# Performance work log

Hardware: AMD Instinct MI355X
Metric: run time of the kernel (lower is better)

The kernel has to match this reference:

```python
import jax, jax.numpy as jnp
import numpy as np

EMB = 768
HEADS = 12
HEAD_DIM = EMB // HEADS  # 64
SCALE = 1.0 / float(np.sqrt(EMB))  # NOTE: source divides by sqrt(emb_size), not sqrt(head_dim)


def setup_inputs() -> dict:
    key = jax.random.key(0)
    k_x, k_wqkv, k_bqkv, k_wp, k_bp = jax.random.split(key, 5)
    b, n = 4, 2048
    x = jax.random.normal(k_x, (b, n, EMB), dtype=jnp.float32)
    # torch Linear default init ~ U(-1/sqrt(in), 1/sqrt(in)); scale doesn't matter for correctness baseline
    lim = 1.0 / np.sqrt(EMB)
    W_qkv = jax.random.uniform(k_wqkv, (EMB, 3 * EMB), minval=-lim, maxval=lim, dtype=jnp.float32)
    b_qkv = jax.random.uniform(k_bqkv, (3 * EMB,), minval=-lim, maxval=lim, dtype=jnp.float32)
    W_proj = jax.random.uniform(k_wp, (EMB, EMB), minval=-lim, maxval=lim, dtype=jnp.float32)
    b_proj = jax.random.uniform(k_bp, (EMB,), minval=-lim, maxval=lim, dtype=jnp.float32)
    return {"x": x, "W_qkv": W_qkv, "b_qkv": b_qkv, "W_proj": W_proj, "b_proj": b_proj}


def reference(x, W_qkv, b_qkv, W_proj, b_proj):
    b, n, _ = x.shape
    qkv = x @ W_qkv + b_qkv                              # [b, n, 3*emb]
    # rearrange 'b n (h d qkv) -> qkv b h n d' : qkv is the innermost split
    qkv = qkv.reshape(b, n, HEADS, HEAD_DIM, 3)
    qkv = jnp.transpose(qkv, (4, 0, 2, 1, 3))            # [3, b, h, n, d]
    q, k, v = qkv[0], qkv[1], qkv[2]
    att = jnp.einsum('bhnd,bhmd->bhnm', q, k) * SCALE    # [b, h, n, n]
    att = jax.nn.softmax(att, axis=-1)
    # dropout is identity at inference
    out = jnp.einsum('bhnm,bhmd->bhnd', att, v)          # [b, h, n, d]
    out = jnp.transpose(out, (0, 2, 1, 3)).reshape(b, n, EMB)  # 'b h n d -> b n (h d)'
    return out @ W_proj + b_proj
```

## Files before the change

### kernel.cpp

```cpp
#include <hip/hip_runtime.h>
#include <math.h>

typedef _Float16 f16x8 __attribute__((ext_vector_type(8)));
typedef _Float16 f16x4 __attribute__((ext_vector_type(4)));
typedef float f32x4 __attribute__((ext_vector_type(4)));
typedef unsigned int uint32;
typedef unsigned short ushort16;

static constexpr int EMB_ = 768;
static constexpr int NH_ = 12;
static constexpr int HD_ = 64;
static constexpr int SEQ_ = 2048;
static constexpr int B_ = 4;
static constexpr float QSCALE_ = 0.036084391824351615f * 1.4426950408889634f;

__device__ __forceinline__ void gload_lds16(const void* g, void* l) {
    __builtin_amdgcn_global_load_lds((const __attribute__((address_space(1))) void*)g,
                                     (__attribute__((address_space(3))) void*)l,
                                     16, 0, 0);
}

__global__ __launch_bounds__(256)
void prep_k(const float* __restrict__ W0, _Float16* __restrict__ Wt0,
            const float* __restrict__ W1, _Float16* __restrict__ Wt1,
            const float* __restrict__ x, _Float16* __restrict__ xh,
            int C0, int C1, int n4)
{
    const int tid = threadIdx.x;
    if (blockIdx.z == 2) {
        const int stride = 72 * 24 * 256;
        for (int i = (blockIdx.y * 72 + blockIdx.x) * 256 + tid; i < n4; i += stride) {
            float4 v = ((const float4*)x)[i];
            f16x4 o = {(_Float16)v.x, (_Float16)v.y, (_Float16)v.z, (_Float16)v.w};
            ((f16x4*)xh)[i] = o;
        }
        return;
    }
    const float* W; _Float16* Wt; int C;
    if (blockIdx.z == 0) { W = W0; Wt = Wt0; C = C0; }
    else                 { W = W1; Wt = Wt1; C = C1; }
    const int c0 = blockIdx.x * 32;
    if (c0 >= C) return;
    const int r0 = blockIdx.y * 32;
    __shared__ float ls[32][33];
    const int tc = tid & 31, tr = tid >> 5;
#pragma unroll
    for (int i = 0; i < 4; ++i)
        ls[tr + 8 * i][tc] = W[(size_t)(r0 + tr + 8 * i) * C + c0 + tc];
    __syncthreads();
#pragma unroll
    for (int i = 0; i < 4; ++i)
        Wt[(size_t)(c0 + tr + 8 * i) * EMB_ + r0 + tc] = (_Float16)ls[tc][tr + 8 * i];
}

template<int EPI>
__global__ __launch_bounds__(256, 2)
void gemm16(const _Float16* __restrict__ A, const _Float16* __restrict__ Bt,
            const float* __restrict__ bias, float* __restrict__ outF,
            _Float16* __restrict__ hq, _Float16* __restrict__ hk,
            _Float16* __restrict__ hv,
            int M, int N, int K)
{
    __shared__ __align__(16) _Float16 As[128 * 64];
    __shared__ __align__(16) _Float16 Bs[128 * 64];

    const int tid  = threadIdx.x;
    const int lane = tid & 63;
    const int w    = tid >> 6;
    const int txm  = lane & 15, g = lane >> 4;
    const int wr   = w >> 1, wc = w & 1;
    const int m0   = blockIdx.y * 128, n0 = blockIdx.x * 128;
    const int nk   = K >> 6;

    const int sr = lane >> 3;
    const int sc = (lane & 7) << 3;
    const _Float16* gA[4]; const _Float16* gB[4];
    _Float16* lA[4]; _Float16* lB[4];
#pragma unroll
    for (int i = 0; i < 4; ++i) {
        const int row = w * 32 + 8 * i;
        gA[i] = A  + (size_t)(m0 + row + sr) * K + sc;
        gB[i] = Bt + (size_t)(n0 + row + sr) * K + sc;
        lA[i] = As + row * 64 + lane * 8;
        lB[i] = Bs + row * 64 + lane * 8;
    }

    f32x4 acc[4][4];
#pragma unroll
    for (int i = 0; i < 4; ++i)
#pragma unroll
        for (int j = 0; j < 4; ++j) acc[i][j] = (f32x4){0.f, 0.f, 0.f, 0.f};

    for (int kt = 0; kt < nk; ++kt) {
        __syncthreads();
#pragma unroll
        for (int i = 0; i < 4; ++i) gload_lds16(gA[i] + kt * 64, lA[i]);
#pragma unroll
        for (int i = 0; i < 4; ++i) gload_lds16(gB[i] + kt * 64, lB[i]);
        __syncthreads();

#pragma unroll
        for (int kh = 0; kh < 2; ++kh) {
            f16x8 af[4], bf[4];
#pragma unroll
            for (int i = 0; i < 4; ++i)
                af[i] = *(const f16x8*)&As[(wr * 64 + 16 * i + txm) * 64 + 32 * kh + 8 * g];
#pragma unroll
            for (int j = 0; j < 4; ++j)
                bf[j] = *(const f16x8*)&Bs[(wc * 64 + 16 * j + txm) * 64 + 32 * kh + 8 * g];
#pragma unroll
            for (int i = 0; i < 4; ++i)
#pragma unroll
                for (int j = 0; j < 4; ++j)
                    acc[i][j] = __builtin_amdgcn_mfma_f32_16x16x32_f16(af[i], bf[j], acc[i][j], 0, 0, 0);
        }
    }

    if (EPI == 0) {
#pragma unroll
        for (int i = 0; i < 4; ++i) {
            const int mB = m0 + wr * 64 + 16 * i + 4 * g;
#pragma unroll
            for (int j = 0; j < 4; ++j) {
                const int n = n0 + wc * 64 + 16 * j + txm;
                const float bv = bias[n];
                const int h   = n / 192;
                const int rem = n - h * 192;
                const int dd  = rem / 3;
                const int s   = rem - dd * 3;
                _Float16* bse = (s == 0) ? hq : (s == 1) ? hk : hv;
                const float scl = (s == 0) ? QSCALE_ : 1.f;
#pragma unroll
                for (int r = 0; r < 4; ++r) {
                    const int mm = mB + r;
                    const int bb = mm >> 11;
                    const int nn = mm & (SEQ_ - 1);
                    const int ddE = (s == 1) ? (dd ^ ((nn & 7) * 8)) : dd;
                    bse[(((size_t)(bb * NH_ + h)) * SEQ_ + nn) * HD_ + ddE] =
                        (_Float16)((acc[i][j][r] + bv) * scl);
                }
            }
        }
    } else {
#pragma unroll
        for (int i = 0; i < 4; ++i) {
#pragma unroll
            for (int r = 0; r < 4; ++r) {
                const int mm = m0 + wr * 64 + 16 * i + 4 * g + r;
                float* dst = outF + (size_t)mm * N + n0 + wc * 64 + txm;
#pragma unroll
                for (int j = 0; j < 4; ++j)
                    dst[16 * j] = acc[i][j][r] + bias[n0 + wc * 64 + 16 * j + txm];
            }
        }
    }
}

__global__ __launch_bounds__(256, 3)
void attn_k(const _Float16* __restrict__ Qb, const _Float16* __restrict__ Kb,
            const _Float16* __restrict__ Vb, _Float16* __restrict__ Out)
{
    __shared__ __align__(16) _Float16 Ks[2][64][64];
    __shared__ __align__(16) _Float16 Vs[2][64][72];

    const int tid  = threadIdx.x;
    const int lane = tid & 63;
    const int wv   = tid >> 6;
    const int txm  = lane & 15;
    const int g    = lane >> 4;

    const int lin  = blockIdx.x;
    const int slot = lin >> 3;
    const int bh   = (lin & 7) + 8 * (slot >> 4);
    const int q0   = (slot & 15) << 7;
    const int bb   = bh / NH_;
    const int hh   = bh - bb * NH_;

    const _Float16* KpB = Kb + (size_t)bh * SEQ_ * HD_;
    const _Float16* VpB = Vb + (size_t)bh * SEQ_ * HD_;

    auto kstage = [&](int buf, int kt) {
        const int c0 = kt << 6;
#pragma unroll
        for (int i = 0; i < 2; ++i)
            gload_lds16(KpB + (size_t)(c0 + 16 * wv + 8 * i) * HD_ + lane * 8,
                        &Ks[buf][16 * wv + 8 * i][0] + lane * 8);
    };

    kstage(0, 0);

    f16x8 qf[2][2];
#pragma unroll
    for (int s = 0; s < 2; ++s)
#pragma unroll
        for (int kh = 0; kh < 2; ++kh)
            qf[s][kh] = *(const f16x8*)(Qb +
                ((size_t)bh * SEQ_ + q0 + 32 * wv + 16 * s + txm) * HD_ + 32 * kh + 8 * g);

    const int vc = (tid & 31) << 1;
    const int vd = (tid >> 5) << 3;
    const int swz = (txm & 7) * 8;

    f32x4 o[2][4];
#pragma unroll
    for (int s = 0; s < 2; ++s)
#pragma unroll
        for (int dt = 0; dt < 4; ++dt) o[s][dt] = (f32x4){0.f, 0.f, 0.f, 0.f};
    float li[2] = {0.f, 0.f};

    uint4 va = *(const uint4*)(VpB + (size_t)vc * HD_ + vd);
    uint4 vb = *(const uint4*)(VpB + (size_t)(vc + 1) * HD_ + vd);

    constexpr int NT = SEQ_ / 64;
    for (int kt = 0; kt < NT; ++kt) {
        const int buf = kt & 1;
        {
            const ushort16* pa = (const ushort16*)&va;
            const ushort16* pb = (const ushort16*)&vb;
#pragma unroll
            for (int j = 0; j < 8; ++j) {
                uint32 wrd = (uint32)pa[j] | ((uint32)pb[j] << 16);
                *(uint32*)&Vs[buf][vd + j][vc] = wrd;
            }
        }
        __syncthreads();

        if (kt + 1 < NT) {
            kstage(buf ^ 1, kt + 1);
            const int c0n = (kt + 1) << 6;
            va = *(const uint4*)(VpB + (size_t)(c0n + vc) * HD_ + vd);
            vb = *(const uint4*)(VpB + (size_t)(c0n + vc + 1) * HD_ + vd);
        }

        f16x8 kf[4][2];
#pragma unroll
        for (int ct = 0; ct < 4; ++ct)
#pragma unroll
            for (int kh = 0; kh < 2; ++kh)
                kf[ct][kh] = *(const f16x8*)&Ks[buf][16 * ct + txm][(32 * kh + 8 * g) ^ swz];

        f32x4 st[2][4];
#pragma unroll
        for (int s = 0; s < 2; ++s)
#pragma unroll
            for (int ct = 0; ct < 4; ++ct) {
                f32x4 a = (f32x4){0.f, 0.f, 0.f, 0.f};
                a = __builtin_amdgcn_mfma_f32_16x16x32_f16(kf[ct][0], qf[s][0], a, 0, 0, 0);
                a = __builtin_amdgcn_mfma_f32_16x16x32_f16(kf[ct][1], qf[s][1], a, 0, 0, 0);
                st[s][ct] = a;
            }

        f16x4 vf[4][4];
#pragma unroll
        for (int dt = 0; dt < 4; ++dt)
#pragma unroll
            for (int ct = 0; ct < 4; ++ct)
                vf[dt][ct] = *(const f16x4*)&Vs[buf][16 * dt + txm][16 * ct + 4 * g];

#pragma unroll
        for (int s = 0; s < 2; ++s) {
            f16x4 pb4[4];
#pragma unroll
            for (int ct = 0; ct < 4; ++ct) {
                float p0 = __builtin_amdgcn_exp2f(st[s][ct][0]);
                float p1 = __builtin_amdgcn_exp2f(st[s][ct][1]);
                float p2 = __builtin_amdgcn_exp2f(st[s][ct][2]);
                float p3 = __builtin_amdgcn_exp2f(st[s][ct][3]);
                li[s] += (p0 + p1) + (p2 + p3);
                pb4[ct] = (f16x4){(_Float16)p0, (_Float16)p1, (_Float16)p2, (_Float16)p3};
            }
#pragma unroll
            for (int dt = 0; dt < 4; ++dt) {
                f32x4 a = o[s][dt];
#pragma unroll
                for (int ct = 0; ct < 4; ++ct)
                    a = __builtin_amdgcn_mfma_f32_16x16x16f16(vf[dt][ct], pb4[ct], a, 0, 0, 0);
                o[s][dt] = a;
            }
        }
    }

#pragma unroll
    for (int s = 0; s < 2; ++s) {
        float rs = li[s];
        rs += __shfl_xor(rs, 16);
        rs += __shfl_xor(rs, 32);
        const float inv = 1.f / rs;
        const int q = q0 + 32 * wv + 16 * s + txm;
        _Float16* dst = Out + ((size_t)bb * SEQ_ + q) * EMB_ + hh * HD_;
#pragma unroll
        for (int dt = 0; dt < 4; ++dt) {
            f16x4 pk = {(_Float16)(o[s][dt][0] * inv), (_Float16)(o[s][dt][1] * inv),
                        (_Float16)(o[s][dt][2] * inv), (_Float16)(o[s][dt][3] * inv)};
            *(f16x4*)(dst + 16 * dt + 4 * g) = pk;
        }
    }
}

extern "C" void kernel_launch(void* const* d_in, const int* in_sizes, int n_in,
                              void* d_out, int out_size, void* d_ws, size_t ws_size,
                              hipStream_t stream)
{
    const float* x    = (const float*)d_in[0];
    const float* Wqkv = (const float*)d_in[1];
    const float* bqkv = (const float*)d_in[2];
    const float* Wp   = (const float*)d_in[3];
    const float* bp   = (const float*)d_in[4];
    float* out = (float*)d_out;

    const size_t PER = (size_t)B_ * NH_ * SEQ_ * HD_;
    _Float16* Qh     = (_Float16*)d_ws;
    _Float16* Kh     = Qh + PER;
    _Float16* Vh     = Kh + PER;
    _Float16* xh     = Vh + PER;
    _Float16* WqkvT  = xh + (size_t)B_ * SEQ_ * EMB_;
    _Float16* WprojT = WqkvT + (size_t)EMB_ * 3 * EMB_;
    _Float16* Ah     = WprojT + (size_t)EMB_ * EMB_;

    const int M = B_ * SEQ_;
    dim3 blk(256);

    prep_k<<<dim3(72, 24, 3), blk, 0, stream>>>(
        Wqkv, WqkvT, Wp, WprojT, x, xh, 3 * EMB_, EMB_, B_ * SEQ_ * EMB_ / 4);

    gemm16<0><<<dim3(3 * EMB_ / 128, M / 128), blk, 0, stream>>>(
        xh, WqkvT, bqkv, nullptr, Qh, Kh, Vh, M, 3 * EMB_, EMB_);

    attn_k<<<dim3((SEQ_ / 128) * B_ * NH_), blk, 0, stream>>>(Qh, Kh, Vh, Ah);

    gemm16<1><<<dim3(EMB_ / 128, M / 128), blk, 0, stream>>>(
        Ah, WprojT, bp, out, nullptr, nullptr, nullptr, M, EMB_, EMB_);
}
```

Baseline: 240.4 us.

## Use two-wave attention blocks with 64 query rows per wave

The attention block shrinks from four waves to two, and each wave now covers 64 query rows as four 16-row subtiles. Each K and V fragment read from LDS is then reused across twice as many query rows, which cuts LDS traffic and fragment loads per unit of MFMA work. The V LDS row stride drops from 72 to 70 halves, and the launch bounds change to (128,2). In exchange, register pressure per wave rises and far fewer waves are resident per CU, so latency hiding gets worse. The new stride also leaves the f16x4 LDS reads only 4-byte aligned.

```diff
diff --git a/kernel.cpp b/kernel.cpp
--- a/kernel.cpp
+++ b/kernel.cpp
@@ -156,12 +156,13 @@
     }
 }
 
-__global__ __launch_bounds__(256, 3)
+#define VSTR 70
+__global__ __launch_bounds__(128, 2)
 void attn_k(const _Float16* __restrict__ Qb, const _Float16* __restrict__ Kb,
             const _Float16* __restrict__ Vb, _Float16* __restrict__ Out)
 {
     __shared__ __align__(16) _Float16 Ks[2][64][64];
-    __shared__ __align__(16) _Float16 Vs[2][64][72];
+    __shared__ __align__(16) _Float16 Vs[2][64][VSTR];
 
     const int tid  = threadIdx.x;
     const int lane = tid & 63;
@@ -182,45 +183,50 @@
     auto kstage = [&](int buf, int kt) {
         const int c0 = kt << 6;
 #pragma unroll
-        for (int i = 0; i < 2; ++i)
-            gload_lds16(KpB + (size_t)(c0 + 16 * wv + 8 * i) * HD_ + lane * 8,
-                        &Ks[buf][16 * wv + 8 * i][0] + lane * 8);
+        for (int i = 0; i < 4; ++i)
+            gload_lds16(KpB + (size_t)(c0 + 32 * wv + 8 * i) * HD_ + lane * 8,
+                        &Ks[buf][32 * wv + 8 * i][0] + lane * 8);
     };
-
     kstage(0, 0);
 
-    f16x8 qf[2][2];
-#pragma unroll
-    for (int s = 0; s < 2; ++s)
+    f16x8 qf[4][2];
+#pragma unroll
+    for (int s = 0; s < 4; ++s)
 #pragma unroll
         for (int kh = 0; kh < 2; ++kh)
             qf[s][kh] = *(const f16x8*)(Qb +
-                ((size_t)bh * SEQ_ + q0 + 32 * wv + 16 * s + txm) * HD_ + 32 * kh + 8 * g);
+                ((size_t)bh * SEQ_ + q0 + 64 * wv + 16 * s + txm) * HD_ + 32 * kh + 8 * g);
 
     const int vc = (tid & 31) << 1;
-    const int vd = (tid >> 5) << 3;
+    const int vd = (tid >> 5) << 4;
     const int swz = (txm & 7) * 8;
 
-    f32x4 o[2][4];
-#pragma unroll
-    for (int s = 0; s < 2; ++s)
+    f32x4 o[4][4];
+#pragma unroll
+    for (int s = 0; s < 4; ++s)
 #pragma unroll
         for (int dt = 0; dt < 4; ++dt) o[s][dt] = (f32x4){0.f, 0.f, 0.f, 0.f};
-    float li[2] = {0.f, 0.f};
-
-    uint4 va = *(const uint4*)(VpB + (size_t)vc * HD_ + vd);
-    uint4 vb = *(const uint4*)(VpB + (size_t)(vc + 1) * HD_ + vd);
+    float li[4] = {0.f, 0.f, 0.f, 0.f};
+
+    uint4 va0 = *(const uint4*)(VpB + (size_t)vc * HD_ + vd);
+    uint4 va1 = *(const uint4*)(VpB + (size_t)vc * HD_ + vd + 8);
+    uint4 vb0 = *(const uint4*)(VpB + (size_t)(vc + 1) * HD_ + vd);
+    uint4 vb1 = *(const uint4*)(VpB + (size_t)(vc + 1) * HD_ + vd + 8);
 
     constexpr int NT = SEQ_ / 64;
     for (int kt = 0; kt < NT; ++kt) {
         const int buf = kt & 1;
         {
-            const ushort16* pa = (const ushort16*)&va;
-            const ushort16* pb = (const ushort16*)&vb;
+            const ushort16* pa0 = (const ushort16*)&va0;
+            const ushort16* pa1 = (const ushort16*)&va1;
+            const ushort16* pb0 = (const ushort16*)&vb0;
+            const ushort16* pb1 = (const ushort16*)&vb1;
 #pragma unroll
             for (int j = 0; j < 8; ++j) {
-                uint32 wrd = (uint32)pa[j] | ((uint32)pb[j] << 16);
-                *(uint32*)&Vs[buf][vd + j][vc] = wrd;
+                *(uint32*)&Vs[buf][vd + j][vc] =
+                    (uint32)pa0[j] | ((uint32)pb0[j] << 16);
+                *(uint32*)&Vs[buf][vd + 8 + j][vc] =
+                    (uint32)pa1[j] | ((uint32)pb1[j] << 16);
             }
         }
         __syncthreads();
@@ -228,8 +234,10 @@
         if (kt + 1 < NT) {
             kstage(buf ^ 1, kt + 1);
             const int c0n = (kt + 1) << 6;
-            va = *(const uint4*)(VpB + (size_t)(c0n + vc) * HD_ + vd);
-            vb = *(const uint4*)(VpB + (size_t)(c0n + vc + 1) * HD_ + vd);
+            va0 = *(const uint4*)(VpB + (size_t)(c0n + vc) * HD_ + vd);
+            va1 = *(const uint4*)(VpB + (size_t)(c0n + vc) * HD_ + vd + 8);
+            vb0 = *(const uint4*)(VpB + (size_t)(c0n + vc + 1) * HD_ + vd);
+            vb1 = *(const uint4*)(VpB + (size_t)(c0n + vc + 1) * HD_ + vd + 8);
         }
 
         f16x8 kf[4][2];
@@ -239,33 +247,30 @@
             for (int kh = 0; kh < 2; ++kh)
                 kf[ct][kh] = *(const f16x8*)&Ks[buf][16 * ct + txm][(32 * kh + 8 * g) ^ swz];
 
-        f32x4 st[2][4];
-#pragma unroll
-        for (int s = 0; s < 2; ++s)
+        f16x4 vf[4][4];
+#pragma unroll
+        for (int dt = 0; dt < 4; ++dt)
+#pragma unroll
+            for (int ct = 0; ct < 4; ++ct)
+                vf[dt][ct] = *(const f16x4*)&Vs[buf][16 * dt + txm][16 * ct + 4 * g];
+
+#pragma unroll
+        for (int s = 0; s < 4; ++s) {
+            f32x4 st[4];
 #pragma unroll
             for (int ct = 0; ct < 4; ++ct) {
                 f32x4 a = (f32x4){0.f, 0.f, 0.f, 0.f};
                 a = __builtin_amdgcn_mfma_f32_16x16x32_f16(kf[ct][0], qf[s][0], a, 0, 0, 0);
                 a = __builtin_amdgcn_mfma_f32_16x16x32_f16(kf[ct][1], qf[s][1], a, 0, 0, 0);
-                st[s][ct] = a;
-            }
-
-        f16x4 vf[4][4];
-#pragma unroll
-        for (int dt = 0; dt < 4; ++dt)
-#pragma unroll
-            for (int ct = 0; ct < 4; ++ct)
-                vf[dt][ct] = *(const f16x4*)&Vs[buf][16 * dt + txm][16 * ct + 4 * g];
-
-#pragma unroll
-        for (int s = 0; s < 2; ++s) {
+                st[ct] = a;
+            }
             f16x4 pb4[4];
 #pragma unroll
             for (int ct = 0; ct < 4; ++ct) {
-                float p0 = __builtin_amdgcn_exp2f(st[s][ct][0]);
-                float p1 = __builtin_amdgcn_exp2f(st[s][ct][1]);
-                float p2 = __builtin_amdgcn_exp2f(st[s][ct][2]);
-                float p3 = __builtin_amdgcn_exp2f(st[s][ct][3]);
+                float p0 = __builtin_amdgcn_exp2f(st[ct][0]);
+                float p1 = __builtin_amdgcn_exp2f(st[ct][1]);
+                float p2 = __builtin_amdgcn_exp2f(st[ct][2]);
+                float p3 = __builtin_amdgcn_exp2f(st[ct][3]);
                 li[s] += (p0 + p1) + (p2 + p3);
                 pb4[ct] = (f16x4){(_Float16)p0, (_Float16)p1, (_Float16)p2, (_Float16)p3};
             }
@@ -281,12 +286,12 @@
     }
 
 #pragma unroll
-    for (int s = 0; s < 2; ++s) {
+    for (int s = 0; s < 4; ++s) {
         float rs = li[s];
         rs += __shfl_xor(rs, 16);
         rs += __shfl_xor(rs, 32);
         const float inv = 1.f / rs;
-        const int q = q0 + 32 * wv + 16 * s + txm;
+        const int q = q0 + 64 * wv + 16 * s + txm;
         _Float16* dst = Out + ((size_t)bb * SEQ_ + q) * EMB_ + hh * HD_;
 #pragma unroll
         for (int dt = 0; dt < 4; ++dt) {
@@ -318,16 +323,15 @@
     _Float16* Ah     = WprojT + (size_t)EMB_ * EMB_;
 
     const int M = B_ * SEQ_;
-    dim3 blk(256);
-
-    prep_k<<<dim3(72, 24, 3), blk, 0, stream>>>(
+
+    prep_k<<<dim3(72, 24, 3), dim3(256), 0, stream>>>(
         Wqkv, WqkvT, Wp, WprojT, x, xh, 3 * EMB_, EMB_, B_ * SEQ_ * EMB_ / 4);
 
-    gemm16<0><<<dim3(3 * EMB_ / 128, M / 128), blk, 0, stream>>>(
+    gemm16<0><<<dim3(3 * EMB_ / 128, M / 128), dim3(256), 0, stream>>>(
         xh, WqkvT, bqkv, nullptr, Qh, Kh, Vh, M, 3 * EMB_, EMB_);
 
-    attn_k<<<dim3((SEQ_ / 128) * B_ * NH_), blk, 0, stream>>>(Qh, Kh, Vh, Ah);
-
-    gemm16<1><<<dim3(EMB_ / 128, M / 128), blk, 0, stream>>>(
+    attn_k<<<dim3((SEQ_ / 128) * B_ * NH_), dim3(128), 0, stream>>>(Qh, Kh, Vh, Ah);
+
+    gemm16<1><<<dim3(EMB_ / 128, M / 128), dim3(256), 0, stream>>>(
         Ah, WprojT, bp, out, nullptr, nullptr, nullptr, M, EMB_, EMB_);
 }
```

After: 257.2 us. 1.07x slower.
